# Optimization experiments

Measured on AMD Instinct MI355X. Metric: run time of the kernel, lower is better.

The kernel has to match this reference:

```python
import jax, jax.numpy as jnp
import numpy as np

D = 1024
HEADS = 16
HEAD_DIM = D // HEADS
B = 4
L = 1024


def setup_inputs() -> dict:
    key = jax.random.key(0)
    kq, kk, kv, kw, kb = jax.random.split(key, 5)
    Q = jax.random.normal(kq, (B, L, D), dtype=jnp.float32)
    K = jax.random.normal(kk, (B, L, D), dtype=jnp.float32)
    V = jax.random.normal(kv, (B, L, D), dtype=jnp.float32)
    # Output projection H: torch nn.Linear(D, D) -> weight (D, D), bias (D,)
    lim = 1.0 / np.sqrt(D)
    W_H = jax.random.uniform(kw, (D, D), minval=-lim, maxval=lim, dtype=jnp.float32)
    b_H = jax.random.uniform(kb, (D,), minval=-lim, maxval=lim, dtype=jnp.float32)
    mask = 0  # falsy -> no masking branch, matching `if mask` in the source
    return {"Q": Q, "K": K, "V": V, "W_H": W_H, "b_H": b_H, "mask": mask}


def reference(Q, K, V, W_H, b_H, mask):
    batch, q_len, _ = Q.shape
    k_len = K.shape[1]
    Qh = Q.reshape(batch, q_len, HEADS, HEAD_DIM)
    Kh = K.reshape(batch, k_len, HEADS, HEAD_DIM)
    Vh = V.reshape(batch, k_len, HEADS, HEAD_DIM)
    scores = jnp.einsum('bqhd,bkhd->bhqk', Qh, Kh)  # [B,H,Lq,Lk]
    if mask:  # mask is a Python scalar (0 -> skip), as in source
        scores = jnp.where(mask == 0, -jnp.inf, scores)
    # NOTE: source scales by sqrt(D), not sqrt(head_dim)
    attn = jax.nn.softmax(scores / np.sqrt(D).astype(np.float32), axis=3)
    out = jnp.einsum('bhql,blhd->bqhd', attn, Vh).reshape(batch, q_len, D)
    return out @ W_H.T + b_H
```

## Files before the change

kernel.cpp:

```cpp
#include <hip/hip_runtime.h>
#include <hip/hip_bf16.h>

typedef __attribute__((ext_vector_type(4))) float f32x4;
typedef __attribute__((ext_vector_type(8))) short bf16x8;
typedef __attribute__((ext_vector_type(4))) short bf16x4;

#if __has_builtin(__builtin_amdgcn_mfma_f32_16x16x16_bf16)
#define MFMA_16x16x16(a, b, c) __builtin_amdgcn_mfma_f32_16x16x16_bf16(a, b, c, 0, 0, 0)
#else
#define MFMA_16x16x16(a, b, c) __builtin_amdgcn_mfma_f32_16x16x16bf16_1k(a, b, c, 0, 0, 0)
#endif

constexpr int Bn  = 4;
constexpr int Ln  = 1024;
constexpr int Dn  = 1024;
constexpr int Hn  = 16;
constexpr int HDn = 64;
constexpr int SEGS = Ln / 64;
constexpr int SEG_SHORTS = 16 * 64 * 4;

static __device__ __forceinline__ unsigned short bf16r(float f) {
    union { float f; unsigned int u; } x;
    x.f = f;
    unsigned int r = x.u + 0x7fffu + ((x.u >> 16) & 1u);
    return (unsigned short)(r >> 16);
}

__global__ __launch_bounds__(256) void prep_kernel(
    const float* __restrict__ Kg, const float* __restrict__ Vg,
    const float* __restrict__ Wg, unsigned short* __restrict__ Kbf,
    unsigned short* __restrict__ Vtg, unsigned short* __restrict__ Wbf)
{
    const int tid = threadIdx.x;
    if (blockIdx.z == 4) {
        const int r0 = blockIdx.x * 64, c0 = blockIdx.y * 64;
        for (int i = 0; i < 4; ++i) {
            int e4 = i * 256 + tid;
            int r = e4 >> 4, c4 = e4 & 15;
            float4 v = *(const float4*)(Wg + (size_t)(r0 + r) * Dn + c0 + c4 * 4);
            ushort4 o;
            o.x = bf16r(v.x); o.y = bf16r(v.y); o.z = bf16r(v.z); o.w = bf16r(v.w);
            *(ushort4*)(Wbf + (size_t)(r0 + r) * Dn + c0 + c4 * 4) = o;
        }
        return;
    }

    __shared__ unsigned short T[64][72];
    const int seg = blockIdx.x;
    const int k0  = seg * 64;
    const int h   = blockIdx.y;
    const int b   = blockIdx.z;
    const float* Kb = Kg + (size_t)b * Ln * Dn + h * HDn;
    const float* Vb = Vg + (size_t)b * Ln * Dn + h * HDn;
    unsigned short* Ko = Kbf + (size_t)b * Ln * Dn + h * HDn;

    for (int i = 0; i < 4; ++i) {
        int e4 = i * 256 + tid;
        int r = e4 >> 4, c4 = e4 & 15;
        float4 kv = *(const float4*)(Kb + (size_t)(k0 + r) * Dn + c4 * 4);
        ushort4 o;
        o.x = bf16r(kv.x); o.y = bf16r(kv.y); o.z = bf16r(kv.z); o.w = bf16r(kv.w);
        *(ushort4*)(Ko + (size_t)(k0 + r) * Dn + c4 * 4) = o;
        float4 vv = *(const float4*)(Vb + (size_t)(k0 + r) * Dn + c4 * 4);
        T[c4 * 4 + 0][r] = bf16r(vv.x);
        T[c4 * 4 + 1][r] = bf16r(vv.y);
        T[c4 * 4 + 2][r] = bf16r(vv.z);
        T[c4 * 4 + 3][r] = bf16r(vv.w);
    }
    __syncthreads();

    unsigned short* out = Vtg + ((size_t)(b * Hn + h) * SEGS + seg) * SEG_SHORTS;
    for (int i = 0; i < 2; ++i) {
        int g = i * 256 + tid;
        int fid = g >> 5, a = g & 31;
        int kn = fid >> 2, dt = fid & 3;
        int L0 = 2 * a, L1 = 2 * a + 1;
        ushort4 lo = *(const ushort4*)&T[dt * 16 + (L0 & 15)][kn * 16 + (L0 >> 4) * 4];
        ushort4 hi = *(const ushort4*)&T[dt * 16 + (L1 & 15)][kn * 16 + (L1 >> 4) * 4];
        union { ushort4 s[2]; uint4 u; } pk;
        pk.s[0] = lo; pk.s[1] = hi;
        *(uint4*)(out + (size_t)g * 8) = pk.u;
    }
}

__global__ __launch_bounds__(256) void attn_kernel(
    const float* __restrict__ Qg, const unsigned short* __restrict__ Kbf,
    const unsigned short* __restrict__ Vtg, unsigned short* __restrict__ Xg)
{
    __shared__ unsigned short Ks[64][72];
    __shared__ unsigned short Vf[SEG_SHORTS];

    const int tid  = threadIdx.x;
    const int wave = tid >> 6;
    const int lane = tid & 63;
    const int l16  = lane & 15;
    const int quad = lane >> 4;

    const int h  = blockIdx.x;
    const int q0 = blockIdx.y * 128;
    const int b  = blockIdx.z;

    const unsigned short* Kb16 = Kbf + (size_t)b * Ln * Dn + h * HDn;
    const unsigned short* Vsegs = Vtg + ((size_t)(b * Hn + h) * SEGS) * SEG_SHORTS;

    bf16x8 aq[2][2];
    for (int set = 0; set < 2; ++set) {
        const float* qp = Qg + ((size_t)b * Ln + q0 + wave * 32 + set * 16 + l16) * Dn
                             + h * HDn + quad * 8;
        float4 a0 = *(const float4*)qp;
        float4 a1 = *(const float4*)(qp + 4);
        float4 a2 = *(const float4*)(qp + 32);
        float4 a3 = *(const float4*)(qp + 36);
        bf16x8 q0v, q1v;
        q0v[0] = (short)bf16r(a0.x); q0v[1] = (short)bf16r(a0.y);
        q0v[2] = (short)bf16r(a0.z); q0v[3] = (short)bf16r(a0.w);
        q0v[4] = (short)bf16r(a1.x); q0v[5] = (short)bf16r(a1.y);
        q0v[6] = (short)bf16r(a1.z); q0v[7] = (short)bf16r(a1.w);
        q1v[0] = (short)bf16r(a2.x); q1v[1] = (short)bf16r(a2.y);
        q1v[2] = (short)bf16r(a2.z); q1v[3] = (short)bf16r(a2.w);
        q1v[4] = (short)bf16r(a3.x); q1v[5] = (short)bf16r(a3.y);
        q1v[6] = (short)bf16r(a3.z); q1v[7] = (short)bf16r(a3.w);
        aq[set][0] = q0v; aq[set][1] = q1v;
    }

    const float SC = 1.4426950408889634f / 32.0f;

    float lsum[2] = {0.f, 0.f};
    f32x4 Oacc[2][4];
    for (int s = 0; s < 2; ++s)
        for (int d = 0; d < 4; ++d) Oacc[s][d] = (f32x4){0.f, 0.f, 0.f, 0.f};

    for (int it = 0; it < SEGS; ++it) {
        const int k0 = it * 64;
        __syncthreads();
        {
            for (int i = 0; i < 2; ++i) {
                int s = i * 256 + tid;
                int r = s >> 3, c8 = s & 7;
                *(uint4*)&Ks[r][c8 * 8] =
                    *(const uint4*)(Kb16 + (size_t)(k0 + r) * Dn + c8 * 8);
            }
            const unsigned short* vsrc = Vsegs + (size_t)it * SEG_SHORTS;
            for (int i = 0; i < 2; ++i) {
                int s = i * 256 + tid;
                *(uint4*)&Vf[s * 8] = *(const uint4*)(vsrc + (size_t)s * 8);
            }
        }
        __syncthreads();

        f32x4 st[2][4];
        for (int n = 0; n < 4; ++n) {
            bf16x8 ka0 = *(const bf16x8*)&Ks[n * 16 + l16][quad * 8];
            bf16x8 ka1 = *(const bf16x8*)&Ks[n * 16 + l16][32 + quad * 8];
            for (int set = 0; set < 2; ++set) {
                f32x4 acc = (f32x4){0.f, 0.f, 0.f, 0.f};
                acc = __builtin_amdgcn_mfma_f32_16x16x32_bf16(ka0, aq[set][0], acc, 0, 0, 0);
                acc = __builtin_amdgcn_mfma_f32_16x16x32_bf16(ka1, aq[set][1], acc, 0, 0, 0);
                st[set][n] = acc;
            }
        }

        bf16x4 pf[2][4];
        for (int set = 0; set < 2; ++set)
            for (int n = 0; n < 4; ++n) {
                float p0 = exp2f(st[set][n][0] * SC);
                float p1 = exp2f(st[set][n][1] * SC);
                float p2 = exp2f(st[set][n][2] * SC);
                float p3 = exp2f(st[set][n][3] * SC);
                lsum[set] += (p0 + p1) + (p2 + p3);
                unsigned int u0 = __float_as_uint(p0) + 0x8000u;
                unsigned int u1 = __float_as_uint(p1) + 0x8000u;
                unsigned int u2 = __float_as_uint(p2) + 0x8000u;
                unsigned int u3 = __float_as_uint(p3) + 0x8000u;
                union { unsigned int u[2]; bf16x4 v; } pk;
                pk.u[0] = __builtin_amdgcn_perm(u1, u0, 0x07060302u);
                pk.u[1] = __builtin_amdgcn_perm(u3, u2, 0x07060302u);
                pf[set][n] = pk.v;
            }

        for (int dt = 0; dt < 4; ++dt)
            for (int kn = 0; kn < 4; ++kn) {
                bf16x4 bv = *(const bf16x4*)&Vf[((kn * 4 + dt) * 64 + lane) * 4];
                Oacc[0][dt] = MFMA_16x16x16(pf[0][kn], bv, Oacc[0][dt]);
                Oacc[1][dt] = MFMA_16x16x16(pf[1][kn], bv, Oacc[1][dt]);
            }
    }

    float linv[2][4];
    for (int set = 0; set < 2; ++set) {
        float rs = lsum[set];
        rs += __shfl_xor(rs, 16, 64);
        rs += __shfl_xor(rs, 32, 64);
        for (int r = 0; r < 4; ++r)
            linv[set][r] = 1.f / __shfl(rs, quad * 4 + r, 64);
    }

    unsigned short* Xb = Xg + ((size_t)b * Ln + q0) * Dn + h * HDn;
    for (int set = 0; set < 2; ++set)
        for (int r = 0; r < 4; ++r) {
            int row = wave * 32 + set * 16 + quad * 4 + r;
            for (int dt = 0; dt < 4; ++dt)
                Xb[(size_t)row * Dn + dt * 16 + l16] =
                    bf16r(Oacc[set][dt][r] * linv[set][r]);
        }
}

__global__ __launch_bounds__(256) void proj_kernel(
    const unsigned short* __restrict__ Xg, const unsigned short* __restrict__ Wbf,
    const float* __restrict__ bg, float* __restrict__ Yg)
{
    __shared__ unsigned short Xs[128][72];
    __shared__ unsigned short Wsh[64][72];

    const int tid  = threadIdx.x;
    const int wave = tid >> 6;
    const int lane = tid & 63;
    const int l16  = lane & 15;
    const int quad = lane >> 4;
    const int mw   = (wave & 1) * 64;
    const int nw   = (wave >> 1) * 32;

    const int n0 = blockIdx.x * 64;
    const int m0 = blockIdx.y * 128;

    f32x4 acc[4][2];
    for (int mt = 0; mt < 4; ++mt)
        for (int nt = 0; nt < 2; ++nt)
            acc[mt][nt] = (f32x4){0.f, 0.f, 0.f, 0.f};

    for (int it = 0; it < Dn / 64; ++it) {
        const int kk0 = it * 64;
        __syncthreads();
        {
            for (int i = 0; i < 4; ++i) {
                int s = i * 256 + tid;
                int r = s >> 3, c8 = s & 7;
                *(uint4*)&Xs[r][c8 * 8] =
                    *(const uint4*)(Xg + (size_t)(m0 + r) * Dn + kk0 + c8 * 8);
            }
            for (int i = 0; i < 2; ++i) {
                int s = i * 256 + tid;
                int r = s >> 3, c8 = s & 7;
                *(uint4*)&Wsh[r][c8 * 8] =
                    *(const uint4*)(Wbf + (size_t)(n0 + r) * Dn + kk0 + c8 * 8);
            }
        }
        __syncthreads();

        bf16x8 af[4][2], bfr[2][2];
        for (int mt = 0; mt < 4; ++mt)
            for (int kk = 0; kk < 2; ++kk)
                af[mt][kk] = *(const bf16x8*)&Xs[mw + mt * 16 + l16][kk * 32 + quad * 8];
        for (int nt = 0; nt < 2; ++nt)
            for (int kk = 0; kk < 2; ++kk)
                bfr[nt][kk] = *(const bf16x8*)&Wsh[nw + nt * 16 + l16][kk * 32 + quad * 8];
        for (int mt = 0; mt < 4; ++mt)
            for (int nt = 0; nt < 2; ++nt) {
                acc[mt][nt] = __builtin_amdgcn_mfma_f32_16x16x32_bf16(
                    af[mt][0], bfr[nt][0], acc[mt][nt], 0, 0, 0);
                acc[mt][nt] = __builtin_amdgcn_mfma_f32_16x16x32_bf16(
                    af[mt][1], bfr[nt][1], acc[mt][nt], 0, 0, 0);
            }
    }

    for (int nt = 0; nt < 2; ++nt) {
        int col = n0 + nw + nt * 16 + l16;
        float bb = bg[col];
        for (int mt = 0; mt < 4; ++mt)
            for (int r = 0; r < 4; ++r) {
                int row = m0 + mw + mt * 16 + quad * 4 + r;
                Yg[(size_t)row * Dn + col] = acc[mt][nt][r] + bb;
            }
    }
}

extern "C" void kernel_launch(void* const* d_in, const int* in_sizes, int n_in,
                              void* d_out, int out_size, void* d_ws, size_t ws_size,
                              hipStream_t stream) {
    const float* Q    = (const float*)d_in[0];
    const float* K    = (const float*)d_in[1];
    const float* V    = (const float*)d_in[2];
    const float* W    = (const float*)d_in[3];
    const float* bias = (const float*)d_in[4];

    unsigned short* Kbf = (unsigned short*)d_ws;
    unsigned short* Vt  = Kbf + (size_t)Bn * Ln * Dn;
    unsigned short* Wbf = Vt  + (size_t)Bn * Ln * Dn;
    unsigned short* X   = Wbf + (size_t)Dn * Dn;
    float* Y = (float*)d_out;

    dim3 gp(SEGS, Hn, Bn + 1);
    prep_kernel<<<gp, 256, 0, stream>>>(K, V, W, Kbf, Vt, Wbf);

    dim3 g1(Hn, Ln / 128, Bn);
    attn_kernel<<<g1, 256, 0, stream>>>(Q, Kbf, Vt, X);

    dim3 g2(Dn / 64, (Bn * Ln) / 128);
    proj_kernel<<<g2, 256, 0, stream>>>(X, Wbf, bias, Y);
}
```

Before: 164.5 us.

## Pre-swizzle K/V into MFMA fragment order and load directly to registers

The prep kernel now writes K and V for each 64-key segment into one contiguous buffer laid out in per-lane MFMA fragment order. The attention kernel drops LDS staging and block barriers and instead loads fragments straight from global memory into registers, prefetching the next segment's K. The softmax scale is folded into Q before the bf16 conversion, and row sums come from an MFMA against a ones vector rather than scalar adds and shuffles. This trades LDS traffic and synchronisation for higher register pressure from a fully unrolled loop and slightly different rounding, since Q is scaled before rounding and the row sum uses bf16-rounded probabilities.

```diff
diff --git a/kernel.cpp b/kernel.cpp
--- a/kernel.cpp
+++ b/kernel.cpp
@@ -17,7 +17,7 @@
 constexpr int Hn  = 16;
 constexpr int HDn = 64;
 constexpr int SEGS = Ln / 64;
-constexpr int SEG_SHORTS = 16 * 64 * 4;
+constexpr int SEG_KV_SHORTS = 8192;
 
 static __device__ __forceinline__ unsigned short bf16r(float f) {
     union { float f; unsigned int u; } x;
@@ -28,8 +28,8 @@
 
 __global__ __launch_bounds__(256) void prep_kernel(
     const float* __restrict__ Kg, const float* __restrict__ Vg,
-    const float* __restrict__ Wg, unsigned short* __restrict__ Kbf,
-    unsigned short* __restrict__ Vtg, unsigned short* __restrict__ Wbf)
+    const float* __restrict__ Wg, unsigned short* __restrict__ KVg,
+    unsigned short* __restrict__ Wbf)
 {
     const int tid = threadIdx.x;
     if (blockIdx.z == 4) {
@@ -45,51 +45,59 @@
         return;
     }
 
-    __shared__ unsigned short T[64][72];
+    __shared__ unsigned short Tk[64][72];
+    __shared__ unsigned short Tv[64][72];
     const int seg = blockIdx.x;
     const int k0  = seg * 64;
     const int h   = blockIdx.y;
     const int b   = blockIdx.z;
     const float* Kb = Kg + (size_t)b * Ln * Dn + h * HDn;
     const float* Vb = Vg + (size_t)b * Ln * Dn + h * HDn;
-    unsigned short* Ko = Kbf + (size_t)b * Ln * Dn + h * HDn;
 
     for (int i = 0; i < 4; ++i) {
         int e4 = i * 256 + tid;
         int r = e4 >> 4, c4 = e4 & 15;
         float4 kv = *(const float4*)(Kb + (size_t)(k0 + r) * Dn + c4 * 4);
-        ushort4 o;
-        o.x = bf16r(kv.x); o.y = bf16r(kv.y); o.z = bf16r(kv.z); o.w = bf16r(kv.w);
-        *(ushort4*)(Ko + (size_t)(k0 + r) * Dn + c4 * 4) = o;
+        Tk[r][c4 * 4 + 0] = bf16r(kv.x);
+        Tk[r][c4 * 4 + 1] = bf16r(kv.y);
+        Tk[r][c4 * 4 + 2] = bf16r(kv.z);
+        Tk[r][c4 * 4 + 3] = bf16r(kv.w);
         float4 vv = *(const float4*)(Vb + (size_t)(k0 + r) * Dn + c4 * 4);
-        T[c4 * 4 + 0][r] = bf16r(vv.x);
-        T[c4 * 4 + 1][r] = bf16r(vv.y);
-        T[c4 * 4 + 2][r] = bf16r(vv.z);
-        T[c4 * 4 + 3][r] = bf16r(vv.w);
+        Tv[c4 * 4 + 0][r] = bf16r(vv.x);
+        Tv[c4 * 4 + 1][r] = bf16r(vv.y);
+        Tv[c4 * 4 + 2][r] = bf16r(vv.z);
+        Tv[c4 * 4 + 3][r] = bf16r(vv.w);
     }
     __syncthreads();
 
-    unsigned short* out = Vtg + ((size_t)(b * Hn + h) * SEGS + seg) * SEG_SHORTS;
+    unsigned short* out = KVg + ((size_t)((b * Hn + h) * SEGS + seg)) * SEG_KV_SHORTS;
     for (int i = 0; i < 2; ++i) {
-        int g = i * 256 + tid;
-        int fid = g >> 5, a = g & 31;
-        int kn = fid >> 2, dt = fid & 3;
-        int L0 = 2 * a, L1 = 2 * a + 1;
-        ushort4 lo = *(const ushort4*)&T[dt * 16 + (L0 & 15)][kn * 16 + (L0 >> 4) * 4];
-        ushort4 hi = *(const ushort4*)&T[dt * 16 + (L1 & 15)][kn * 16 + (L1 >> 4) * 4];
-        union { ushort4 s[2]; uint4 u; } pk;
-        pk.s[0] = lo; pk.s[1] = hi;
-        *(uint4*)(out + (size_t)g * 8) = pk.u;
+        int s = i * 256 + tid;
+        int fid = s >> 6, L = s & 63;
+        int l16s = L & 15, qd = L >> 4;
+        {
+            int n = fid >> 1, half = fid & 1;
+            ushort4 lo = *(const ushort4*)&Tk[n * 16 + l16s][half * 32 + qd * 8];
+            ushort4 hi = *(const ushort4*)&Tk[n * 16 + l16s][half * 32 + qd * 8 + 4];
+            union { ushort4 s[2]; uint4 u; } pk;
+            pk.s[0] = lo; pk.s[1] = hi;
+            *(uint4*)(out + (size_t)s * 8) = pk.u;
+        }
+        {
+            int dt = fid >> 1, knp = fid & 1;
+            ushort4 lo = *(const ushort4*)&Tv[dt * 16 + l16s][knp * 32 + qd * 4];
+            ushort4 hi = *(const ushort4*)&Tv[dt * 16 + l16s][knp * 32 + 16 + qd * 4];
+            union { ushort4 s[2]; uint4 u; } pk;
+            pk.s[0] = lo; pk.s[1] = hi;
+            *(uint4*)(out + 4096 + (size_t)s * 8) = pk.u;
+        }
     }
 }
 
 __global__ __launch_bounds__(256) void attn_kernel(
-    const float* __restrict__ Qg, const unsigned short* __restrict__ Kbf,
-    const unsigned short* __restrict__ Vtg, unsigned short* __restrict__ Xg)
+    const float* __restrict__ Qg, const unsigned short* __restrict__ KVg,
+    unsigned short* __restrict__ Xg)
 {
-    __shared__ unsigned short Ks[64][72];
-    __shared__ unsigned short Vf[SEG_SHORTS];
-
     const int tid  = threadIdx.x;
     const int wave = tid >> 6;
     const int lane = tid & 63;
@@ -100,8 +108,10 @@
     const int q0 = blockIdx.y * 128;
     const int b  = blockIdx.z;
 
-    const unsigned short* Kb16 = Kbf + (size_t)b * Ln * Dn + h * HDn;
-    const unsigned short* Vsegs = Vtg + ((size_t)(b * Hn + h) * SEGS) * SEG_SHORTS;
+    const unsigned short* kvb =
+        KVg + (size_t)(b * Hn + h) * SEGS * SEG_KV_SHORTS + (size_t)lane * 8;
+
+    const float SC = 1.4426950408889634f / 32.0f;
 
     bf16x8 aq[2][2];
     for (int set = 0; set < 2; ++set) {
@@ -112,46 +122,50 @@
         float4 a2 = *(const float4*)(qp + 32);
         float4 a3 = *(const float4*)(qp + 36);
         bf16x8 q0v, q1v;
-        q0v[0] = (short)bf16r(a0.x); q0v[1] = (short)bf16r(a0.y);
-        q0v[2] = (short)bf16r(a0.z); q0v[3] = (short)bf16r(a0.w);
-        q0v[4] = (short)bf16r(a1.x); q0v[5] = (short)bf16r(a1.y);
-        q0v[6] = (short)bf16r(a1.z); q0v[7] = (short)bf16r(a1.w);
-        q1v[0] = (short)bf16r(a2.x); q1v[1] = (short)bf16r(a2.y);
-        q1v[2] = (short)bf16r(a2.z); q1v[3] = (short)bf16r(a2.w);
-        q1v[4] = (short)bf16r(a3.x); q1v[5] = (short)bf16r(a3.y);
-        q1v[6] = (short)bf16r(a3.z); q1v[7] = (short)bf16r(a3.w);
+        q0v[0] = (short)bf16r(a0.x * SC); q0v[1] = (short)bf16r(a0.y * SC);
+        q0v[2] = (short)bf16r(a0.z * SC); q0v[3] = (short)bf16r(a0.w * SC);
+        q0v[4] = (short)bf16r(a1.x * SC); q0v[5] = (short)bf16r(a1.y * SC);
+        q0v[6] = (short)bf16r(a1.z * SC); q0v[7] = (short)bf16r(a1.w * SC);
+        q1v[0] = (short)bf16r(a2.x * SC); q1v[1] = (short)bf16r(a2.y * SC);
+        q1v[2] = (short)bf16r(a2.z * SC); q1v[3] = (short)bf16r(a2.w * SC);
+        q1v[4] = (short)bf16r(a3.x * SC); q1v[5] = (short)bf16r(a3.y * SC);
+        q1v[6] = (short)bf16r(a3.z * SC); q1v[7] = (short)bf16r(a3.w * SC);
         aq[set][0] = q0v; aq[set][1] = q1v;
     }
 
-    const float SC = 1.4426950408889634f / 32.0f;
-
-    float lsum[2] = {0.f, 0.f};
-    f32x4 Oacc[2][4];
-    for (int s = 0; s < 2; ++s)
+    const bf16x4 ones = (bf16x4){(short)0x3F80, (short)0x3F80,
+                                 (short)0x3F80, (short)0x3F80};
+
+    f32x4 Oacc[2][4], Osum[2];
+    for (int s = 0; s < 2; ++s) {
+        Osum[s] = (f32x4){0.f, 0.f, 0.f, 0.f};
         for (int d = 0; d < 4; ++d) Oacc[s][d] = (f32x4){0.f, 0.f, 0.f, 0.f};
-
+    }
+
+    bf16x8 ka[2][4][2];
+    bf16x8 vv[4][2];
+
+    for (int n = 0; n < 4; ++n)
+        for (int hf = 0; hf < 2; ++hf)
+            ka[0][n][hf] = *(const bf16x8*)(kvb + (n * 2 + hf) * 512);
+
+#pragma unroll
     for (int it = 0; it < SEGS; ++it) {
-        const int k0 = it * 64;
-        __syncthreads();
-        {
-            for (int i = 0; i < 2; ++i) {
-                int s = i * 256 + tid;
-                int r = s >> 3, c8 = s & 7;
-                *(uint4*)&Ks[r][c8 * 8] =
-                    *(const uint4*)(Kb16 + (size_t)(k0 + r) * Dn + c8 * 8);
-            }
-            const unsigned short* vsrc = Vsegs + (size_t)it * SEG_SHORTS;
-            for (int i = 0; i < 2; ++i) {
-                int s = i * 256 + tid;
-                *(uint4*)&Vf[s * 8] = *(const uint4*)(vsrc + (size_t)s * 8);
-            }
-        }
-        __syncthreads();
+        const int cur = it & 1, nxt = cur ^ 1;
+        const unsigned short* segp = kvb + (size_t)it * SEG_KV_SHORTS;
+
+        for (int dt = 0; dt < 4; ++dt)
+            for (int knp = 0; knp < 2; ++knp)
+                vv[dt][knp] = *(const bf16x8*)(segp + 4096 + (dt * 2 + knp) * 512);
+
+        for (int n = 0; n < 4; ++n)
+            for (int hf = 0; hf < 2; ++hf)
+                ka[nxt][n][hf] =
+                    *(const bf16x8*)(segp + SEG_KV_SHORTS + (n * 2 + hf) * 512);
 
         f32x4 st[2][4];
         for (int n = 0; n < 4; ++n) {
-            bf16x8 ka0 = *(const bf16x8*)&Ks[n * 16 + l16][quad * 8];
-            bf16x8 ka1 = *(const bf16x8*)&Ks[n * 16 + l16][32 + quad * 8];
+            bf16x8 ka0 = ka[cur][n][0], ka1 = ka[cur][n][1];
             for (int set = 0; set < 2; ++set) {
                 f32x4 acc = (f32x4){0.f, 0.f, 0.f, 0.f};
                 acc = __builtin_amdgcn_mfma_f32_16x16x32_bf16(ka0, aq[set][0], acc, 0, 0, 0);
@@ -163,11 +177,10 @@
         bf16x4 pf[2][4];
         for (int set = 0; set < 2; ++set)
             for (int n = 0; n < 4; ++n) {
-                float p0 = exp2f(st[set][n][0] * SC);
-                float p1 = exp2f(st[set][n][1] * SC);
-                float p2 = exp2f(st[set][n][2] * SC);
-                float p3 = exp2f(st[set][n][3] * SC);
-                lsum[set] += (p0 + p1) + (p2 + p3);
+                float p0 = exp2f(st[set][n][0]);
+                float p1 = exp2f(st[set][n][1]);
+                float p2 = exp2f(st[set][n][2]);
+                float p3 = exp2f(st[set][n][3]);
                 unsigned int u0 = __float_as_uint(p0) + 0x8000u;
                 unsigned int u1 = __float_as_uint(p1) + 0x8000u;
                 unsigned int u2 = __float_as_uint(p2) + 0x8000u;
@@ -178,30 +191,30 @@
                 pf[set][n] = pk.v;
             }
 
+        for (int set = 0; set < 2; ++set)
+            for (int kn = 0; kn < 4; ++kn)
+                Osum[set] = MFMA_16x16x16(pf[set][kn], ones, Osum[set]);
+
         for (int dt = 0; dt < 4; ++dt)
-            for (int kn = 0; kn < 4; ++kn) {
-                bf16x4 bv = *(const bf16x4*)&Vf[((kn * 4 + dt) * 64 + lane) * 4];
-                Oacc[0][dt] = MFMA_16x16x16(pf[0][kn], bv, Oacc[0][dt]);
-                Oacc[1][dt] = MFMA_16x16x16(pf[1][kn], bv, Oacc[1][dt]);
-            }
-    }
-
-    float linv[2][4];
-    for (int set = 0; set < 2; ++set) {
-        float rs = lsum[set];
-        rs += __shfl_xor(rs, 16, 64);
-        rs += __shfl_xor(rs, 32, 64);
-        for (int r = 0; r < 4; ++r)
-            linv[set][r] = 1.f / __shfl(rs, quad * 4 + r, 64);
+            for (int knp = 0; knp < 2; ++knp) {
+                bf16x8 v8 = vv[dt][knp];
+                bf16x4 lo = __builtin_shufflevector(v8, v8, 0, 1, 2, 3);
+                bf16x4 hi = __builtin_shufflevector(v8, v8, 4, 5, 6, 7);
+                for (int set = 0; set < 2; ++set) {
+                    Oacc[set][dt] = MFMA_16x16x16(pf[set][knp * 2], lo, Oacc[set][dt]);
+                    Oacc[set][dt] = MFMA_16x16x16(pf[set][knp * 2 + 1], hi, Oacc[set][dt]);
+                }
+            }
     }
 
     unsigned short* Xb = Xg + ((size_t)b * Ln + q0) * Dn + h * HDn;
     for (int set = 0; set < 2; ++set)
         for (int r = 0; r < 4; ++r) {
+            float linv = 1.f / Osum[set][r];
             int row = wave * 32 + set * 16 + quad * 4 + r;
             for (int dt = 0; dt < 4; ++dt)
                 Xb[(size_t)row * Dn + dt * 16 + l16] =
-                    bf16r(Oacc[set][dt][r] * linv[set][r]);
+                    bf16r(Oacc[set][dt][r] * linv);
         }
 }
 
@@ -283,17 +296,17 @@
     const float* W    = (const float*)d_in[3];
     const float* bias = (const float*)d_in[4];
 
-    unsigned short* Kbf = (unsigned short*)d_ws;
-    unsigned short* Vt  = Kbf + (size_t)Bn * Ln * Dn;
-    unsigned short* Wbf = Vt  + (size_t)Bn * Ln * Dn;
+    const size_t KV_SHORTS = (size_t)Bn * Hn * SEGS * SEG_KV_SHORTS;
+    unsigned short* KV  = (unsigned short*)d_ws;
+    unsigned short* Wbf = KV + KV_SHORTS + 16384;
     unsigned short* X   = Wbf + (size_t)Dn * Dn;
     float* Y = (float*)d_out;
 
     dim3 gp(SEGS, Hn, Bn + 1);
-    prep_kernel<<<gp, 256, 0, stream>>>(K, V, W, Kbf, Vt, Wbf);
+    prep_kernel<<<gp, 256, 0, stream>>>(K, V, W, KV, Wbf);
 
     dim3 g1(Hn, Ln / 128, Bn);
-    attn_kernel<<<g1, 256, 0, stream>>>(Q, Kbf, Vt, X);
+    attn_kernel<<<g1, 256, 0, stream>>>(Q, KV, X);
 
     dim3 g2(Dn / 64, (Bn * Ln) / 128);
     proj_kernel<<<g2, 256, 0, stream>>>(X, Wbf, bias, Y);
```

New measurement: 166.2 us. No clear change (+1.0%).
